# Performance work log

Hardware: AMD Instinct MI355X
Metric: run time of the kernel (lower is better)

The kernel has to match this reference:

```python
import jax, jax.numpy as jnp
import numpy as np

LAMBDA_REG = 1.0  # default lambda_reg in MetaOptNetHead_Ridge_CS


def setup_inputs() -> dict:
    key = jax.random.key(0)
    k1, k2, k3 = jax.random.split(key, 3)
    B, n_query, n_support, d = 512, 75, 25, 1024
    n_way, n_shot = 5, 5
    query = jax.random.normal(k1, (B, n_query, d), dtype=jnp.float32)
    support = jax.random.normal(k2, (B, n_support, d), dtype=jnp.float32)
    support_labels = jax.random.randint(k3, (B, n_support), 0, n_way, dtype=jnp.int64)
    scale = jnp.ones((1,), dtype=jnp.float32)
    return {
        "query": query,
        "support": support,
        "support_labels": support_labels,
        "scale": scale,
        "n_way": n_way,
        "n_shot": n_shot,
    }


def reference(query, support, support_labels, scale, n_way, n_shot):
    # query:   (B, n_query, d)
    # support: (B, n_support, d), n_support == n_way * n_shot
    B, n_support, d = support.shape
    dtype = support.dtype
    # one-hot support labels: (B, n_support, n_way)
    Y = jax.nn.one_hot(support_labels, n_way, dtype=dtype)
    # K = S S^T + lambda I : (B, n_support, n_support)
    K = jnp.einsum("bnd,bmd->bnm", support, support) \
        + LAMBDA_REG * jnp.eye(n_support, dtype=dtype)
    # close_w = S^T K^{-1} Y  (computed via batched solve instead of explicit inverse)
    A = jnp.linalg.solve(K, Y)                    # (B, n_support, n_way)
    W = jnp.einsum("bnd,bnc->bdc", support, A)    # (B, d, n_way)
    logits = jnp.einsum("bqd,bdc->bqc", query, W)  # (B, n_query, n_way)
    return scale * logits
```

## Files before the change

### kernel.cpp

```cpp
#include <hip/hip_runtime.h>
#include <hip/hip_bf16.h>

#define NS 25
#define NW 5
#define D  1024
#define NQ 75
#define SPAD 132

__device__ __forceinline__ void async_ld16(const float* gsrc, float* ldst) {
    __builtin_amdgcn_global_load_lds(
        (const __attribute__((address_space(1))) void*)gsrc,
        (__attribute__((address_space(3))) void*)ldst, 16, 0, 0);
}

__global__ __launch_bounds__(256) void k_solve(const float* __restrict__ S,
                                               const int* __restrict__ labels,
                                               float* __restrict__ A_ws) {
    const int b = blockIdx.x;
    const int t = threadIdx.x;

    __shared__ float s_chunk[2][NS * SPAD];
    __shared__ float kpart[8][NS * NS];
    __shared__ float M[NS * 33];
    __shared__ float prow[32];
    __shared__ float pcol[NS];

    const float4* Sb4 = (const float4*)(S + (size_t)b * NS * D);

    float4 r0, r1, r2, r3 = make_float4(0.f, 0.f, 0.f, 0.f);
    auto LOADC = [&](int ch) {
        r0 = Sb4[((t      ) >> 5) * 256 + ch * 32 + ((t      ) & 31)];
        r1 = Sb4[((t + 256) >> 5) * 256 + ch * 32 + ((t + 256) & 31)];
        r2 = Sb4[((t + 512) >> 5) * 256 + ch * 32 + ((t + 512) & 31)];
        if (t < 32) r3 = Sb4[((t + 768) >> 5) * 256 + ch * 32 + ((t + 768) & 31)];
    };
    auto WRITEC = [&](int bb) {
        *(float4*)&s_chunk[bb][((t      ) >> 5) * SPAD + ((t      ) & 31) * 4] = r0;
        *(float4*)&s_chunk[bb][((t + 256) >> 5) * SPAD + ((t + 256) & 31) * 4] = r1;
        *(float4*)&s_chunk[bb][((t + 512) >> 5) * SPAD + ((t + 512) & 31) * 4] = r2;
        if (t < 32)
            *(float4*)&s_chunk[bb][((t + 768) >> 5) * SPAD + ((t + 768) & 31) * 4] = r3;
    };

    const int tile = t >> 3;
    const int sk   = t & 7;
    const int ti = (tile < 5) ? 0 : (tile < 9) ? 1 : (tile < 12) ? 2 : (tile < 14) ? 3 : 4;
    const int tbase = (ti == 0) ? 0 : (ti == 1) ? 5 : (ti == 2) ? 9 : (ti == 3) ? 12 : 14;
    const int tj = ti + (tile - tbase);
    const int i0 = ti * 5, j0 = tj * 5;
    float acc[5][5] = {};

    LOADC(0); WRITEC(0); LOADC(1);
    asm volatile("s_waitcnt lgkmcnt(0)" ::: "memory");
    __builtin_amdgcn_s_barrier();

    for (int ch = 0; ch < 8; ++ch) {
        if (t < 120) {
            const float* sc_ = s_chunk[ch & 1];
#pragma unroll
            for (int ii = 0; ii < 4; ++ii) {
                const int kl = sk * 4 + ii * 32;
                float4 si[5], sj[5];
#pragma unroll
                for (int a = 0; a < 5; ++a) si[a] = *(const float4*)&sc_[(i0 + a) * SPAD + kl];
#pragma unroll
                for (int c = 0; c < 5; ++c) sj[c] = *(const float4*)&sc_[(j0 + c) * SPAD + kl];
#pragma unroll
                for (int a = 0; a < 5; ++a)
#pragma unroll
                    for (int c = 0; c < 5; ++c)
                        acc[a][c] += si[a].x * sj[c].x + si[a].y * sj[c].y +
                                     si[a].z * sj[c].z + si[a].w * sj[c].w;
            }
        }
        if (ch + 1 < 8) WRITEC((ch + 1) & 1);
        if (ch + 2 < 8) LOADC(ch + 2);
        asm volatile("s_waitcnt lgkmcnt(0)" ::: "memory");
        __builtin_amdgcn_s_barrier();
    }

    if (t < 120) {
#pragma unroll
        for (int a = 0; a < 5; ++a)
#pragma unroll
            for (int c = 0; c < 5; ++c)
                kpart[sk][(i0 + a) * NS + (j0 + c)] = acc[a][c];
    }
    __syncthreads();

    for (int item = t; item < NS * NS; item += 256) {
        const int i = item / NS, j = item % NS;
        const int ii = min(i, j), jj = max(i, j);
        float s = 0.f;
#pragma unroll
        for (int p = 0; p < 8; ++p) s += kpart[p][ii * NS + jj];
        if (i == j) s += 1.0f;
        M[i * 33 + j] = s;
    }
    if (t < NS * NW) {
        const int i = t / NW, c = t % NW;
        M[i * 33 + NS + c] = (labels[b * NS + i] == c) ? 1.f : 0.f;
    }
    __syncthreads();

    for (int p = 0; p < NS; ++p) {
        if (t < 30) prow[t] = M[p * 33 + t];
        if (t >= 32 && t < 32 + NS) pcol[t - 32] = M[(t - 32) * 33 + p];
        __syncthreads();
        const float finv = 1.0f / prow[p];
        for (int item = t; item < NS * 30; item += 256) {
            const int rr = item / 30, cc = item % 30;
            if (rr == p) M[rr * 33 + cc] = prow[cc] * finv;
            else         M[rr * 33 + cc] = M[rr * 33 + cc] - pcol[rr] * finv * prow[cc];
        }
        __syncthreads();
    }

    if (t < NS * NW)
        A_ws[(size_t)b * NS * NW + t] = M[(t / NW) * 33 + NS + (t % NW)];
}

__global__ __launch_bounds__(320) void k_logits(const float* __restrict__ Q,
                                                const float* __restrict__ S,
                                                const float* __restrict__ A_ws,
                                                const float* __restrict__ scale,
                                                float* __restrict__ out) {
    const int b = blockIdx.x;
    const int t = threadIdx.x;
    const int wbase = t & ~63;
    const int l = t & 63;
    const int w = t >> 6;

    __shared__ float4 qt[2][1280];
    __shared__ float  Wl[NW * 1024];
    __shared__ float  A_s[128];
    __shared__ float  outbuf[NQ * NW];
    __shared__ float  scsh;

    float* qtf = (float*)qt;
    const float4* Sb4 = (const float4*)(S + (size_t)b * NS * D);
    const float4* Qb4 = (const float4*)(Q + (size_t)b * NQ * D);

    if (t < NS * NW) A_s[t] = A_ws[(size_t)b * NS * NW + t];
    if (t == 0) scsh = scale[0];
    __syncthreads();

    auto dma_s = [&](int ch, int bb) {
#pragma unroll
        for (int it = 0; it < 3; ++it) {
            int g = it * 320 + t;
            int gc = (g < 800) ? g : 799;
            const float* src = (const float*)&Sb4[(gc >> 5) * 256 + ch * 32 + (gc & 31)];
            float* dst = qtf + bb * 3840 + (it * 320 + wbase) * 4;
            async_ld16(src, dst);
        }
    };

    dma_s(0, 0); dma_s(1, 1);
    for (int ch = 0; ch < 8; ++ch) {
        if (ch < 7) asm volatile("s_waitcnt vmcnt(3)" ::: "memory");
        else        asm volatile("s_waitcnt vmcnt(0)" ::: "memory");
        __builtin_amdgcn_s_barrier();
        const float* sc_ = qtf + (ch & 1) * 3840;
#pragma unroll
        for (int it = 0; it < 2; ++it) {
            const int item = it * 320 + t;
            const int c = item >> 7, kl = item & 127;
            float sum = 0.f;
#pragma unroll
            for (int j = 0; j < NS; ++j) sum += A_s[j * NW + c] * sc_[j * 128 + kl];
            Wl[c * 1024 + ch * 128 + kl] = sum;
        }
        asm volatile("s_waitcnt lgkmcnt(0)" ::: "memory");
        __builtin_amdgcn_s_barrier();
        if (ch + 2 < 8) dma_s(ch + 2, ch & 1);
    }

    auto dma_q = [&](int tp, int bb) {
#pragma unroll
        for (int it = 0; it < 4; ++it) {
            int g = it * 320 + t;
            const float* src = (const float*)&Qb4[(tp * 5 + (g >> 8)) * 256 + (g & 255)];
            float* dst = (float*)qt[bb] + (it * 320 + wbase) * 4;
            async_ld16(src, dst);
        }
    };

    dma_q(0, 0); dma_q(1, 1);
    const float4* WL4 = (const float4*)Wl;
    const float4* W0 = WL4, *W1 = WL4 + 256, *W2 = WL4 + 512, *W3 = WL4 + 768, *W4 = WL4 + 1024;

    for (int tp = 0; tp < 15; ++tp) {
        if (tp < 14) asm volatile("s_waitcnt vmcnt(4)" ::: "memory");
        else         asm volatile("s_waitcnt vmcnt(0)" ::: "memory");
        __builtin_amdgcn_s_barrier();
        const float4* qr = qt[tp & 1] + w * 256;
        float a0 = 0.f, a1 = 0.f, a2 = 0.f, a3 = 0.f, a4 = 0.f;
#pragma unroll
        for (int i = 0; i < 4; ++i) {
            const int o = i * 64 + l;
            const float4 qv = qr[o];
            const float4 w0 = W0[o], w1 = W1[o], w2 = W2[o], w3 = W3[o], w4 = W4[o];
            a0 += qv.x * w0.x + qv.y * w0.y + qv.z * w0.z + qv.w * w0.w;
            a1 += qv.x * w1.x + qv.y * w1.y + qv.z * w1.z + qv.w * w1.w;
            a2 += qv.x * w2.x + qv.y * w2.y + qv.z * w2.z + qv.w * w2.w;
            a3 += qv.x * w3.x + qv.y * w3.y + qv.z * w3.z + qv.w * w3.w;
            a4 += qv.x * w4.x + qv.y * w4.y + qv.z * w4.z + qv.w * w4.w;
        }
#pragma unroll
        for (int m = 32; m >= 1; m >>= 1) {
            a0 += __shfl_xor(a0, m);
            a1 += __shfl_xor(a1, m);
            a2 += __shfl_xor(a2, m);
            a3 += __shfl_xor(a3, m);
            a4 += __shfl_xor(a4, m);
        }
        if (l == 0) {
            const int r = tp * 5 + w;
            outbuf[r * NW + 0] = a0; outbuf[r * NW + 1] = a1; outbuf[r * NW + 2] = a2;
            outbuf[r * NW + 3] = a3; outbuf[r * NW + 4] = a4;
        }
        __builtin_amdgcn_s_barrier();
        if (tp + 2 < 15) dma_q(tp + 2, tp & 1);
    }

    __syncthreads();
    const float scv = scsh;
    for (int i = t; i < NQ * NW; i += 320)
        out[(size_t)b * NQ * NW + i] = outbuf[i] * scv;
}

extern "C" void kernel_launch(void* const* d_in, const int* in_sizes, int n_in,
                              void* d_out, int out_size, void* d_ws, size_t ws_size,
                              hipStream_t stream) {
    const float* Q      = (const float*)d_in[0];
    const float* S      = (const float*)d_in[1];
    const int*   labels = (const int*)d_in[2];
    const float* scale  = (const float*)d_in[3];
    const int B = in_sizes[1] / (NS * D);

    float* A_ws = (float*)d_ws;

    k_solve<<<B, 256, 0, stream>>>(S, labels, A_ws);
    k_logits<<<B, 320, 0, stream>>>(Q, S, A_ws, scale, (float*)d_out);
}
```

Baseline: 303.1 us.

## Rewrite logits kernel with register-held W, direct query loads, and DPP reductions

The logits kernel now uses 512 threads. It builds W in registers from direct global loads of S using float4 outer products, instead of the LDS-DMA chunked pipeline. Each wave keeps its W slice in registers and streams query rows straight from global memory through a triple-buffered register prefetch with explicit vmcnt waits. The shuffle reductions are replaced with DPP row operations. This removes LDS staging and barriers per query tile, but adds register pressure and relies on hand-counted waitcnts and DPP control codes being correct.

```diff
diff --git a/kernel.cpp b/kernel.cpp
--- a/kernel.cpp
+++ b/kernel.cpp
@@ -7,11 +7,14 @@
 #define NQ 75
 #define SPAD 132
 
-__device__ __forceinline__ void async_ld16(const float* gsrc, float* ldst) {
-    __builtin_amdgcn_global_load_lds(
-        (const __attribute__((address_space(1))) void*)gsrc,
-        (__attribute__((address_space(3))) void*)ldst, 16, 0, 0);
-}
+#define DPP_ADD(x, CTRL, RM) do {                                              \
+    int _s = __builtin_amdgcn_update_dpp(0, __builtin_bit_cast(int, (x)),      \
+                                         (CTRL), (RM), 0xF, true);             \
+    (x) += __builtin_bit_cast(float, _s); } while (0)
+#define RED64(x) do {                                                          \
+    DPP_ADD(x, 0x111, 0xF); DPP_ADD(x, 0x112, 0xF);                            \
+    DPP_ADD(x, 0x114, 0xF); DPP_ADD(x, 0x118, 0xF);                            \
+    DPP_ADD(x, 0x142, 0xA); DPP_ADD(x, 0x143, 0x8); } while (0)
 
 __global__ __launch_bounds__(256) void k_solve(const float* __restrict__ S,
                                                const int* __restrict__ labels,
@@ -120,113 +123,94 @@
         A_ws[(size_t)b * NS * NW + t] = M[(t / NW) * 33 + NS + (t % NW)];
 }
 
-__global__ __launch_bounds__(320) void k_logits(const float* __restrict__ Q,
-                                                const float* __restrict__ S,
-                                                const float* __restrict__ A_ws,
-                                                const float* __restrict__ scale,
-                                                float* __restrict__ out) {
+__global__ __launch_bounds__(512, 3) void k_logits(const float* __restrict__ Q,
+                                                   const float* __restrict__ S,
+                                                   const float* __restrict__ A_ws,
+                                                   const float* __restrict__ scale,
+                                                   float* __restrict__ out) {
     const int b = blockIdx.x;
     const int t = threadIdx.x;
-    const int wbase = t & ~63;
     const int l = t & 63;
     const int w = t >> 6;
 
-    __shared__ float4 qt[2][1280];
-    __shared__ float  Wl[NW * 1024];
-    __shared__ float  A_s[128];
+    __shared__ float4 Wsh4[NW * 256];
+    __shared__ float  A_s[NS * NW];
     __shared__ float  outbuf[NQ * NW];
     __shared__ float  scsh;
 
-    float* qtf = (float*)qt;
-    const float4* Sb4 = (const float4*)(S + (size_t)b * NS * D);
-    const float4* Qb4 = (const float4*)(Q + (size_t)b * NQ * D);
-
     if (t < NS * NW) A_s[t] = A_ws[(size_t)b * NS * NW + t];
     if (t == 0) scsh = scale[0];
     __syncthreads();
 
-    auto dma_s = [&](int ch, int bb) {
-#pragma unroll
-        for (int it = 0; it < 3; ++it) {
-            int g = it * 320 + t;
-            int gc = (g < 800) ? g : 799;
-            const float* src = (const float*)&Sb4[(gc >> 5) * 256 + ch * 32 + (gc & 31)];
-            float* dst = qtf + bb * 3840 + (it * 320 + wbase) * 4;
-            async_ld16(src, dst);
-        }
-    };
-
-    dma_s(0, 0); dma_s(1, 1);
-    for (int ch = 0; ch < 8; ++ch) {
-        if (ch < 7) asm volatile("s_waitcnt vmcnt(3)" ::: "memory");
-        else        asm volatile("s_waitcnt vmcnt(0)" ::: "memory");
-        __builtin_amdgcn_s_barrier();
-        const float* sc_ = qtf + (ch & 1) * 3840;
-#pragma unroll
-        for (int it = 0; it < 2; ++it) {
-            const int item = it * 320 + t;
-            const int c = item >> 7, kl = item & 127;
-            float sum = 0.f;
-#pragma unroll
-            for (int j = 0; j < NS; ++j) sum += A_s[j * NW + c] * sc_[j * 128 + kl];
-            Wl[c * 1024 + ch * 128 + kl] = sum;
-        }
-        asm volatile("s_waitcnt lgkmcnt(0)" ::: "memory");
-        __builtin_amdgcn_s_barrier();
-        if (ch + 2 < 8) dma_s(ch + 2, ch & 1);
-    }
-
-    auto dma_q = [&](int tp, int bb) {
-#pragma unroll
-        for (int it = 0; it < 4; ++it) {
-            int g = it * 320 + t;
-            const float* src = (const float*)&Qb4[(tp * 5 + (g >> 8)) * 256 + (g & 255)];
-            float* dst = (float*)qt[bb] + (it * 320 + wbase) * 4;
-            async_ld16(src, dst);
-        }
-    };
-
-    dma_q(0, 0); dma_q(1, 1);
-    const float4* WL4 = (const float4*)Wl;
-    const float4* W0 = WL4, *W1 = WL4 + 256, *W2 = WL4 + 512, *W3 = WL4 + 768, *W4 = WL4 + 1024;
-
-    for (int tp = 0; tp < 15; ++tp) {
-        if (tp < 14) asm volatile("s_waitcnt vmcnt(4)" ::: "memory");
-        else         asm volatile("s_waitcnt vmcnt(0)" ::: "memory");
-        __builtin_amdgcn_s_barrier();
-        const float4* qr = qt[tp & 1] + w * 256;
+    if (t < 256) {
+        const float4* S4 = (const float4*)(S + (size_t)b * NS * D);
+        float4 wa0 = {0,0,0,0}, wa1 = {0,0,0,0}, wa2 = {0,0,0,0}, wa3 = {0,0,0,0}, wa4 = {0,0,0,0};
+#pragma unroll
+        for (int j = 0; j < NS; ++j) {
+            const float4 sv = S4[j * 256 + t];
+            const float a0 = A_s[j * NW + 0], a1 = A_s[j * NW + 1], a2 = A_s[j * NW + 2];
+            const float a3 = A_s[j * NW + 3], a4 = A_s[j * NW + 4];
+            wa0.x += a0 * sv.x; wa0.y += a0 * sv.y; wa0.z += a0 * sv.z; wa0.w += a0 * sv.w;
+            wa1.x += a1 * sv.x; wa1.y += a1 * sv.y; wa1.z += a1 * sv.z; wa1.w += a1 * sv.w;
+            wa2.x += a2 * sv.x; wa2.y += a2 * sv.y; wa2.z += a2 * sv.z; wa2.w += a2 * sv.w;
+            wa3.x += a3 * sv.x; wa3.y += a3 * sv.y; wa3.z += a3 * sv.z; wa3.w += a3 * sv.w;
+            wa4.x += a4 * sv.x; wa4.y += a4 * sv.y; wa4.z += a4 * sv.z; wa4.w += a4 * sv.w;
+        }
+        Wsh4[0 * 256 + t] = wa0; Wsh4[1 * 256 + t] = wa1; Wsh4[2 * 256 + t] = wa2;
+        Wsh4[3 * 256 + t] = wa3; Wsh4[4 * 256 + t] = wa4;
+    }
+    __syncthreads();
+
+    float4 W4[NW][4];
+#pragma unroll
+    for (int c = 0; c < NW; ++c)
+#pragma unroll
+        for (int s = 0; s < 4; ++s)
+            W4[c][s] = Wsh4[c * 256 + l + 64 * s];
+
+    const float4* Qb4 = (const float4*)(Q + (size_t)b * NQ * D);
+    float4 qA[4], qB[4], qC[4];
+
+    auto ISSUE = [&](float4* qv, int i) {
+        int rr = w + 8 * i; if (rr > 74) rr -= 8;
+        const float4* p = Qb4 + rr * 256 + l;
+        qv[0] = p[0]; qv[1] = p[64]; qv[2] = p[128]; qv[3] = p[192];
+    };
+    auto BODY = [&](const float4* qv, int i) {
         float a0 = 0.f, a1 = 0.f, a2 = 0.f, a3 = 0.f, a4 = 0.f;
 #pragma unroll
-        for (int i = 0; i < 4; ++i) {
-            const int o = i * 64 + l;
-            const float4 qv = qr[o];
-            const float4 w0 = W0[o], w1 = W1[o], w2 = W2[o], w3 = W3[o], w4 = W4[o];
-            a0 += qv.x * w0.x + qv.y * w0.y + qv.z * w0.z + qv.w * w0.w;
-            a1 += qv.x * w1.x + qv.y * w1.y + qv.z * w1.z + qv.w * w1.w;
-            a2 += qv.x * w2.x + qv.y * w2.y + qv.z * w2.z + qv.w * w2.w;
-            a3 += qv.x * w3.x + qv.y * w3.y + qv.z * w3.z + qv.w * w3.w;
-            a4 += qv.x * w4.x + qv.y * w4.y + qv.z * w4.z + qv.w * w4.w;
-        }
-#pragma unroll
-        for (int m = 32; m >= 1; m >>= 1) {
-            a0 += __shfl_xor(a0, m);
-            a1 += __shfl_xor(a1, m);
-            a2 += __shfl_xor(a2, m);
-            a3 += __shfl_xor(a3, m);
-            a4 += __shfl_xor(a4, m);
-        }
-        if (l == 0) {
-            const int r = tp * 5 + w;
-            outbuf[r * NW + 0] = a0; outbuf[r * NW + 1] = a1; outbuf[r * NW + 2] = a2;
-            outbuf[r * NW + 3] = a3; outbuf[r * NW + 4] = a4;
-        }
-        __builtin_amdgcn_s_barrier();
-        if (tp + 2 < 15) dma_q(tp + 2, tp & 1);
-    }
+        for (int s = 0; s < 4; ++s) {
+            const float4 q = qv[s];
+            a0 += q.x * W4[0][s].x + q.y * W4[0][s].y + q.z * W4[0][s].z + q.w * W4[0][s].w;
+            a1 += q.x * W4[1][s].x + q.y * W4[1][s].y + q.z * W4[1][s].z + q.w * W4[1][s].w;
+            a2 += q.x * W4[2][s].x + q.y * W4[2][s].y + q.z * W4[2][s].z + q.w * W4[2][s].w;
+            a3 += q.x * W4[3][s].x + q.y * W4[3][s].y + q.z * W4[3][s].z + q.w * W4[3][s].w;
+            a4 += q.x * W4[4][s].x + q.y * W4[4][s].y + q.z * W4[4][s].z + q.w * W4[4][s].w;
+        }
+        RED64(a0); RED64(a1); RED64(a2); RED64(a3); RED64(a4);
+        if (l == 63) {
+            int rr = w + 8 * i; if (rr > 74) rr -= 8;
+            outbuf[rr * NW + 0] = a0; outbuf[rr * NW + 1] = a1; outbuf[rr * NW + 2] = a2;
+            outbuf[rr * NW + 3] = a3; outbuf[rr * NW + 4] = a4;
+        }
+    };
+#define WAITV(N) asm volatile("s_waitcnt vmcnt(" #N ")" ::: "memory")
+
+    ISSUE(qA, 0); ISSUE(qB, 1); ISSUE(qC, 2);
+    WAITV(8);  BODY(qA, 0); ISSUE(qA, 3);
+    WAITV(8);  BODY(qB, 1); ISSUE(qB, 4);
+    WAITV(8);  BODY(qC, 2); ISSUE(qC, 5);
+    WAITV(8);  BODY(qA, 3); ISSUE(qA, 6);
+    WAITV(8);  BODY(qB, 4); ISSUE(qB, 7);
+    WAITV(8);  BODY(qC, 5); ISSUE(qC, 8);
+    WAITV(8);  BODY(qA, 6); ISSUE(qA, 9);
+    WAITV(8);  BODY(qB, 7);
+    WAITV(4);  BODY(qC, 8);
+    WAITV(0);  BODY(qA, 9);
 
     __syncthreads();
     const float scv = scsh;
-    for (int i = t; i < NQ * NW; i += 320)
+    for (int i = t; i < NQ * NW; i += 512)
         out[(size_t)b * NQ * NW + i] = outbuf[i] * scv;
 }
 
@@ -242,5 +226,5 @@
     float* A_ws = (float*)d_ws;
 
     k_solve<<<B, 256, 0, stream>>>(S, labels, A_ws);
-    k_logits<<<B, 320, 0, stream>>>(Q, S, A_ws, scale, (float*)d_out);
+    k_logits<<<B, 512, 0, stream>>>(Q, S, A_ws, scale, (float*)d_out);
 }
```

After: 285.9 us. 1.06x faster.
